# Optimization experiments

Measured on AMD Instinct MI355X. Metric: run time of the kernel, lower is better.

## Reference

```python
import jax, jax.numpy as jnp
import numpy as np

EMBED = 1024
B, S = 8, 2048

def setup_inputs() -> dict:
    key = jax.random.key(0)
    k1, k2 = jax.random.split(key)
    x = jax.random.normal(k1, (B, S, EMBED), dtype=jnp.float32)
    # torch Linear(embed, 3*embed): store weight already transposed as [E, 3E]
    W_qkv = jax.random.normal(k2, (EMBED, 3 * EMBED), dtype=jnp.float32) * (1.0 / np.sqrt(EMBED))
    b_qkv = jnp.zeros((3 * EMBED,), dtype=jnp.float32)
    return {"x": x, "W_qkv": W_qkv, "b_qkv": b_qkv}

def reference(x, W_qkv, b_qkv):
    E = x.shape[-1]
    qkv = x @ W_qkv + b_qkv                      # [B,S,3E]
    Q, K, V = jnp.split(qkv, 3, axis=-1)         # each [B,S,E]
    scale = 1.0 / jnp.sqrt(jnp.asarray(E, x.dtype))
    scores = jnp.einsum('bqe,bke->bqk', Q, K) * scale  # [B,S,S]
    attn = jax.nn.softmax(scores, axis=-1)
    return jnp.einsum('bqk,bke->bqe', attn, V)   # [B,S,E]
```

## Files before the change

kernel.cpp:

```cpp
#include <hip/hip_runtime.h>

typedef unsigned short u16;
typedef unsigned int u32;
typedef __attribute__((ext_vector_type(8))) short short8;
typedef __attribute__((ext_vector_type(4))) short short4v;
typedef __attribute__((ext_vector_type(4))) float f32x4;

__device__ __forceinline__ u16 f2bf(float f) {
    u32 u = __float_as_uint(f);
    u32 r = (u + 0x7fffu + ((u >> 16) & 1u)) >> 16;
    return (u16)r;
}
__device__ __forceinline__ float bf2f(u16 h) {
    return __uint_as_float(((u32)h) << 16);
}

__device__ __forceinline__ void gload_lds16(const void* g, void* l) {
    __builtin_amdgcn_global_load_lds((const __attribute__((address_space(1))) void*)g,
                                     (__attribute__((address_space(3))) void*)l, 16, 0, 0);
}

#define BARRIER() do { __builtin_amdgcn_sched_barrier(0); __builtin_amdgcn_s_barrier(); __builtin_amdgcn_sched_barrier(0); } while (0)
#define VMCNT(N)  asm volatile("s_waitcnt vmcnt(" #N ")" ::: "memory")

#define STAGE(ptr, LDG, LOFF, RBASE, kelem) \
    do { gload_lds16((ptr) + (size_t)(RBASE) * (LDG) + (kelem),        lds + (LOFF) + ((RBASE) + (wid << 3)) * 128); \
         gload_lds16((ptr) + (size_t)((RBASE) + 64) * (LDG) + (kelem), lds + (LOFF) + ((RBASE) + 64 + (wid << 3)) * 128); } while (0)

template<int ROFF, int QH>
__device__ __forceinline__ void ld_a(short8 (&a)[4][2], const char* lds, int arow, int c0, int c1) {
    #pragma unroll
    for (int mf = 0; mf < 4; ++mf) {
        a[mf][0] = *(const short8*)(lds + ROFF + QH * 16384 + mf * 2048 + arow + c0);
        a[mf][1] = *(const short8*)(lds + ROFF + QH * 16384 + mf * 2048 + arow + c1);
    }
}
template<int ROFF, int QH>
__device__ __forceinline__ void ld_b(short8 (&b)[2][2], const char* lds, int brow, int c0, int c1) {
    #pragma unroll
    for (int nf = 0; nf < 2; ++nf) {
        b[nf][0] = *(const short8*)(lds + ROFF + QH * 16384 + nf * 2048 + brow + c0);
        b[nf][1] = *(const short8*)(lds + ROFF + QH * 16384 + nf * 2048 + brow + c1);
    }
}

template<int QM, int QN>
__device__ __forceinline__ void mfq(f32x4 (&acc)[2][4][2][2], short8 (&a)[4][2], short8 (&b)[2][2]) {
    __builtin_amdgcn_s_setprio(1);
    #pragma unroll
    for (int mf = 0; mf < 4; ++mf)
        #pragma unroll
        for (int nf = 0; nf < 2; ++nf) {
            acc[QM][mf][QN][nf] = __builtin_amdgcn_mfma_f32_16x16x32_bf16(a[mf][0], b[nf][0], acc[QM][mf][QN][nf], 0, 0, 0);
            acc[QM][mf][QN][nf] = __builtin_amdgcn_mfma_f32_16x16x32_bf16(a[mf][1], b[nf][1], acc[QM][mf][QN][nf], 0, 0, 0);
        }
    __builtin_amdgcn_s_setprio(0);
}

template<int EPI, int LDA, int LDB, int LDC, int K>
__global__ __launch_bounds__(512, 2)
void gemm8p(const u16* __restrict__ A, long long sA,
            const u16* __restrict__ B, long long sB,
            void* __restrict__ Cv, long long sC,
            const float* __restrict__ bias, float* __restrict__ ps,
            u16* __restrict__ vt, float scale, int GX, int GY)
{
    extern __shared__ char lds[];
    const int tid  = threadIdx.x;
    const int wid  = tid >> 6;
    const int lane = tid & 63;

    const int nwg = gridDim.x;
    int bid = blockIdx.x;
    bid = (bid & 7) * (nwg >> 3) + (bid >> 3);
    const int bx  = bid % GX;
    const int rem = bid / GX;
    const int by  = rem % GY;
    const long long z = rem / GY;

    const int bm = by * 256, bn = bx * 256;
    const u16* Atile = A + z * sA + (size_t)bm * LDA;
    const u16* Btile = B + z * sB + (size_t)bn * LDB;

    const int wm = wid >> 2, wn = wid & 3;
    const int l15   = lane & 15;
    const int lxor  = (lane & 7) << 4;
    const int khi   = (lane >> 4) << 4;
    const int colk0 = khi ^ lxor;
    const int colk1 = (64 + khi) ^ lxor;
    const int arow  = (wm * 64 + l15) * 128;
    const int brow  = (wn * 32 + l15) * 128;

    const int swz = ((lane & 7) ^ (lane >> 3)) << 3;
    const u16* pA = Atile + (size_t)((wid << 3) + (lane >> 3)) * LDA + swz;
    const u16* pB = Btile + (size_t)((wid << 3) + (lane >> 3)) * LDB + swz;

    f32x4 acc[2][4][2][2];
    #pragma unroll
    for (int i = 0; i < 2; ++i)
        #pragma unroll
        for (int m = 0; m < 4; ++m)
            #pragma unroll
            for (int j = 0; j < 2; ++j)
                #pragma unroll
                for (int n = 0; n < 2; ++n)
                    acc[i][m][j][n] = (f32x4){0.f, 0.f, 0.f, 0.f};

    STAGE(pA, LDA, 0,     0,   0);  STAGE(pA, LDA, 0,     128, 0);
    STAGE(pB, LDB, 32768, 0,   0);  STAGE(pB, LDB, 32768, 128, 0);
    STAGE(pA, LDA, 65536, 0,   64);
    STAGE(pB, LDB, 98304, 0,   64); STAGE(pB, LDB, 98304, 128, 64);
    VMCNT(6);
    BARRIER();

    short8 a[4][2], b0[2][2], b1[2][2];
    const int NI = K >> 7;

    for (int it = 0; it < NI; ++it) {
        const bool more = (it + 1 < NI);
        const int kc1 = it * 128 + 64;
        const int kn  = it * 128 + 128;
        const int kn2 = kn + 64;

        ld_a<0, 0>(a, lds, arow, colk0, colk1);
        ld_b<32768, 0>(b0, lds, brow, colk0, colk1);
        STAGE(pA, LDA, 65536, 128, kc1);
        BARRIER(); mfq<0, 0>(acc, a, b0);
        ld_b<32768, 1>(b1, lds, brow, colk0, colk1);
        BARRIER(); mfq<0, 1>(acc, a, b1);
        ld_a<0, 1>(a, lds, arow, colk0, colk1);
        if (more) STAGE(pB, LDB, 32768, 0, kn);
        BARRIER(); mfq<1, 1>(acc, a, b1);
        if (more) { STAGE(pB, LDB, 32768, 128, kn); VMCNT(4); }
        else      { VMCNT(0); }
        BARRIER(); mfq<1, 0>(acc, a, b0);
        ld_a<65536, 0>(a, lds, arow, colk0, colk1);
        ld_b<98304, 0>(b0, lds, brow, colk0, colk1);
        if (more) STAGE(pA, LDA, 0, 0, kn);
        BARRIER(); mfq<0, 0>(acc, a, b0);
        ld_b<98304, 1>(b1, lds, brow, colk0, colk1);
        if (more) STAGE(pA, LDA, 0, 128, kn);
        BARRIER(); mfq<0, 1>(acc, a, b1);
        ld_a<65536, 1>(a, lds, arow, colk0, colk1);
        if (more) { STAGE(pB, LDB, 98304, 0, kn2); STAGE(pB, LDB, 98304, 128, kn2); }
        BARRIER(); mfq<1, 1>(acc, a, b1);
        if (more) STAGE(pA, LDA, 65536, 0, kn2);
        VMCNT(6);
        BARRIER(); mfq<1, 0>(acc, a, b0);
    }

    const int r0 = (lane >> 4) * 4;
    const int cc = lane & 15;

    if (EPI == 3) {
        BARRIER();
        float* rs = (float*)lds;
        u16* C = (u16*)Cv + z * sC;
        float rsum[2][4][4];
        #pragma unroll
        for (int qm = 0; qm < 2; ++qm)
            #pragma unroll
            for (int mf = 0; mf < 4; ++mf)
                #pragma unroll
                for (int r = 0; r < 4; ++r) rsum[qm][mf][r] = 0.f;
        #pragma unroll
        for (int qn = 0; qn < 2; ++qn)
            #pragma unroll
            for (int nf = 0; nf < 2; ++nf) {
                const int col = bn + qn * 128 + wn * 32 + nf * 16 + cc;
                #pragma unroll
                for (int qm = 0; qm < 2; ++qm)
                    #pragma unroll
                    for (int mf = 0; mf < 4; ++mf) {
                        const int row = bm + qm * 128 + wm * 64 + mf * 16 + r0;
                        #pragma unroll
                        for (int r = 0; r < 4; ++r) {
                            const float e = __expf(acc[qm][mf][qn][nf][r] * scale);
                            const u16 eb = f2bf(e);
                            C[(size_t)(row + r) * LDC + col] = eb;
                            rsum[qm][mf][r] += bf2f(eb);
                        }
                    }
            }
        #pragma unroll
        for (int qm = 0; qm < 2; ++qm)
            #pragma unroll
            for (int mf = 0; mf < 4; ++mf)
                #pragma unroll
                for (int r = 0; r < 4; ++r) {
                    float v = rsum[qm][mf][r];
                    v += __shfl_xor(v, 1); v += __shfl_xor(v, 2);
                    v += __shfl_xor(v, 4); v += __shfl_xor(v, 8);
                    if (cc == 0)
                        rs[wn * 256 + qm * 128 + wm * 64 + mf * 16 + r0 + r] = v;
                }
        __syncthreads();
        if (tid < 256) {
            const float s = rs[tid] + rs[256 + tid] + rs[512 + tid] + rs[768 + tid];
            ps[((size_t)z * 2048 + bm + tid) * GX + bx] = s;
        }
        return;
    }

    if (EPI == 0 && bn >= 2048) {
        #pragma unroll
        for (int qn = 0; qn < 2; ++qn)
            #pragma unroll
            for (int nf = 0; nf < 2; ++nf) {
                const int col = bn + qn * 128 + wn * 32 + nf * 16 + cc;
                const float badd = bias[col];
                const int e = col - 2048;
                #pragma unroll
                for (int qm = 0; qm < 2; ++qm)
                    #pragma unroll
                    for (int mf = 0; mf < 4; ++mf) {
                        const int row = bm + qm * 128 + wm * 64 + mf * 16 + r0;
                        short4v o;
                        #pragma unroll
                        for (int r = 0; r < 4; ++r)
                            o[r] = (short)f2bf(acc[qm][mf][qn][nf][r] + badd);
                        *(short4v*)&vt[((size_t)(row >> 11) << 21) + (size_t)e * 2048 + (row & 2047)] = o;
                    }
            }
        return;
    }

    #pragma unroll
    for (int qn = 0; qn < 2; ++qn)
        #pragma unroll
        for (int nf = 0; nf < 2; ++nf) {
            const int col = bn + qn * 128 + wn * 32 + nf * 16 + cc;
            const float badd = (EPI == 0) ? bias[col] : 0.f;
            #pragma unroll
            for (int qm = 0; qm < 2; ++qm)
                #pragma unroll
                for (int mf = 0; mf < 4; ++mf) {
                    const int row = bm + qm * 128 + wm * 64 + mf * 16 + r0;
                    #pragma unroll
                    for (int r = 0; r < 4; ++r) {
                        if (EPI == 4) {
                            const float v = acc[qm][mf][qn][nf][r] * scale *
                                            bias[(size_t)z * 2048 + row + r];
                            ((float*)Cv + z * sC)[(size_t)(row + r) * LDC + col] = v;
                        } else {
                            const float v = acc[qm][mf][qn][nf][r] * scale + badd;
                            ((u16*)Cv + z * sC)[(size_t)(row + r) * LDC + col] = f2bf(v);
                        }
                    }
                }
        }
}

__global__ __launch_bounds__(256)
void denom_inv(const float* __restrict__ Ps, float* __restrict__ dinv, int n)
{
    const int i = blockIdx.x * 256 + threadIdx.x;
    if (i >= n) return;
    const float* p = Ps + (size_t)i * 8;
    const float s = ((p[0] + p[1]) + (p[2] + p[3])) + ((p[4] + p[5]) + (p[6] + p[7]));
    dinv[i] = 1.0f / s;
}

__global__ __launch_bounds__(256)
void cvt_f32_bf16(const float* __restrict__ in, u16* __restrict__ out, int n8)
{
    const int i = blockIdx.x * 256 + threadIdx.x;
    if (i >= n8) return;
    const float4* p = (const float4*)in;
    const float4 a = p[2 * i], b = p[2 * i + 1];
    short8 o;
    o[0] = (short)f2bf(a.x); o[1] = (short)f2bf(a.y);
    o[2] = (short)f2bf(a.z); o[3] = (short)f2bf(a.w);
    o[4] = (short)f2bf(b.x); o[5] = (short)f2bf(b.y);
    o[6] = (short)f2bf(b.z); o[7] = (short)f2bf(b.w);
    ((short8*)out)[i] = o;
}

__global__ __launch_bounds__(256)
void cvt_w_t(const float* __restrict__ W, u16* __restrict__ Wt)
{
    __shared__ u16 T[32][33];
    const int tid = threadIdx.x;
    const int tr = tid >> 3;
    const int tc = (tid & 7) * 4;
    const int c0 = blockIdx.x * 32;
    const int r0 = blockIdx.y * 32;
    const float4 v = *(const float4*)&W[(size_t)(r0 + tr) * 3072 + c0 + tc];
    T[tr][tc + 0] = f2bf(v.x); T[tr][tc + 1] = f2bf(v.y);
    T[tr][tc + 2] = f2bf(v.z); T[tr][tc + 3] = f2bf(v.w);
    __syncthreads();
    short4v o;
    o[0] = (short)T[tc + 0][tr]; o[1] = (short)T[tc + 1][tr];
    o[2] = (short)T[tc + 2][tr]; o[3] = (short)T[tc + 3][tr];
    *(short4v*)&Wt[(size_t)(c0 + tr) * 1024 + r0 + tc] = o;
}

extern "C" void kernel_launch(void* const* d_in, const int* in_sizes, int n_in,
                              void* d_out, int out_size, void* d_ws, size_t ws_size,
                              hipStream_t stream) {
    const float* x    = (const float*)d_in[0];
    const float* W    = (const float*)d_in[1];
    const float* bias = (const float*)d_in[2];
    float* out = (float*)d_out;

    const int B = 8, S = 2048, E = 1024, N3 = 3072;
    const int M = B * S;

    char* ws = (char*)d_ws;
    u16* xb   = (u16*)ws;
    u16* Wtb  = (u16*)(ws + 33554432);
    u16* qkvb = (u16*)(ws + 39845888);
    u16* Vtb  = (u16*)(ws + 140509184);
    u16* Sb   = (u16*)(ws + 174063616);

    const size_t sbFull = (size_t)B * S * S * 2;
    const size_t sbOne  = (size_t)S * S * 2;
    const size_t psFull = (size_t)M * 8 * sizeof(float);
    const size_t need_full = 174063616ull + sbFull + psFull + (size_t)M * sizeof(float);
    const bool full = ws_size >= need_full;

    float* Ps   = (float*)(ws + 174063616 + (full ? sbFull : sbOne));
    float* dinv = Ps + (full ? (size_t)M * 8 : (size_t)S * 8);

    const float sc = 1.0f / 32.0f;
    const int LDSB = 131072;

    auto kQKV = gemm8p<0, 1024, 1024, 3072, 1024>;
    auto kQKT = gemm8p<3, 3072, 3072, 2048, 1024>;
    auto kPV  = gemm8p<4, 2048, 2048, 1024, 2048>;
    (void)hipFuncSetAttribute(reinterpret_cast<const void*>(kQKV),
                              hipFuncAttributeMaxDynamicSharedMemorySize, LDSB);
    (void)hipFuncSetAttribute(reinterpret_cast<const void*>(kQKT),
                              hipFuncAttributeMaxDynamicSharedMemorySize, LDSB);
    (void)hipFuncSetAttribute(reinterpret_cast<const void*>(kPV),
                              hipFuncAttributeMaxDynamicSharedMemorySize, LDSB);

    cvt_f32_bf16<<<dim3((M * E) / 8 / 256), 256, 0, stream>>>(x, xb, (M * E) / 8);
    cvt_w_t<<<dim3(96, 32), 256, 0, stream>>>(W, Wtb);

    kQKV<<<dim3(12 * 64), 512, LDSB, stream>>>(xb, 0, Wtb, 0, qkvb, 0,
                                               bias, nullptr, Vtb, 1.0f, 12, 64);

    if (full) {
        kQKT<<<dim3(8 * 8 * 8), 512, LDSB, stream>>>(
            qkvb, (long long)S * N3, qkvb + E, (long long)S * N3,
            Sb, (long long)S * S, nullptr, Ps, nullptr, sc, 8, 8);
        denom_inv<<<dim3(M / 256), 256, 0, stream>>>(Ps, dinv, M);
        kPV<<<dim3(4 * 8 * 8), 512, LDSB, stream>>>(
            Sb, (long long)S * S, Vtb, (long long)E * S,
            out, (long long)S * E, dinv, nullptr, nullptr, 1.0f, 4, 8);
    } else {
        for (int b = 0; b < B; ++b) {
            const u16* Qb = qkvb + (size_t)b * S * N3;
            kQKT<<<dim3(8 * 8), 512, LDSB, stream>>>(
                Qb, 0, Qb + E, 0, Sb, 0, nullptr, Ps, nullptr, sc, 8, 8);
            denom_inv<<<dim3(S / 256), 256, 0, stream>>>(Ps, dinv, S);
            kPV<<<dim3(4 * 8), 512, LDSB, stream>>>(
                Sb, 0, Vtb + (size_t)b * E * S, 0,
                out + (size_t)b * S * E, 0, dinv, nullptr, nullptr, 1.0f, 4, 8);
        }
    }
}
```

Measured before the change: 266.4 us.

## Restructure GEMM main loop from eight to four barrier phases per iteration

The GEMM main loop is reorganized so that each 128-wide K iteration has four barrier-separated phases instead of eight. Each phase now issues two MFMA quadrants back to back, and the global-to-LDS staging loads and vmcnt waits are reordered to match. The aim is to cut barrier synchronization overhead and give the scheduler longer MFMA runs. The cost is less interleaving of LDS reads with compute and a changed prefetch distance, which could expose load latency or create LDS hazards if the wait counts are wrong.

```diff
diff --git a/kernel.cpp b/kernel.cpp
--- a/kernel.cpp
+++ b/kernel.cpp
@@ -59,7 +59,7 @@
 
 template<int EPI, int LDA, int LDB, int LDC, int K>
 __global__ __launch_bounds__(512, 2)
-void gemm8p(const u16* __restrict__ A, long long sA,
+void gemm4p(const u16* __restrict__ A, long long sA,
             const u16* __restrict__ B, long long sB,
             void* __restrict__ Cv, long long sC,
             const float* __restrict__ bias, float* __restrict__ ps,
@@ -108,9 +108,8 @@
 
     STAGE(pA, LDA, 0,     0,   0);  STAGE(pA, LDA, 0,     128, 0);
     STAGE(pB, LDB, 32768, 0,   0);  STAGE(pB, LDB, 32768, 128, 0);
-    STAGE(pA, LDA, 65536, 0,   64);
-    STAGE(pB, LDB, 98304, 0,   64); STAGE(pB, LDB, 98304, 128, 64);
-    VMCNT(6);
+    STAGE(pA, LDA, 65536, 0,   64); STAGE(pB, LDB, 98304, 0,   64);
+    VMCNT(4);
     BARRIER();
 
     short8 a[4][2], b0[2][2], b1[2][2];
@@ -124,29 +123,26 @@
 
         ld_a<0, 0>(a, lds, arow, colk0, colk1);
         ld_b<32768, 0>(b0, lds, brow, colk0, colk1);
-        STAGE(pA, LDA, 65536, 128, kc1);
-        BARRIER(); mfq<0, 0>(acc, a, b0);
         ld_b<32768, 1>(b1, lds, brow, colk0, colk1);
-        BARRIER(); mfq<0, 1>(acc, a, b1);
+        STAGE(pB, LDB, 98304, 128, kc1); STAGE(pA, LDA, 65536, 128, kc1);
+        VMCNT(8);
+        BARRIER();
+        mfq<0, 0>(acc, a, b0); mfq<0, 1>(acc, a, b1);
         ld_a<0, 1>(a, lds, arow, colk0, colk1);
-        if (more) STAGE(pB, LDB, 32768, 0, kn);
-        BARRIER(); mfq<1, 1>(acc, a, b1);
-        if (more) { STAGE(pB, LDB, 32768, 128, kn); VMCNT(4); }
-        else      { VMCNT(0); }
-        BARRIER(); mfq<1, 0>(acc, a, b0);
+        if (more) { STAGE(pA, LDA, 0, 0, kn); STAGE(pB, LDB, 32768, 0, kn); }
+        BARRIER();
+        mfq<1, 1>(acc, a, b1); mfq<1, 0>(acc, a, b0);
         ld_a<65536, 0>(a, lds, arow, colk0, colk1);
         ld_b<98304, 0>(b0, lds, brow, colk0, colk1);
-        if (more) STAGE(pA, LDA, 0, 0, kn);
-        BARRIER(); mfq<0, 0>(acc, a, b0);
         ld_b<98304, 1>(b1, lds, brow, colk0, colk1);
-        if (more) STAGE(pA, LDA, 0, 128, kn);
-        BARRIER(); mfq<0, 1>(acc, a, b1);
+        if (more) { STAGE(pB, LDB, 32768, 128, kn); STAGE(pA, LDA, 0, 128, kn); VMCNT(8); }
+        else      { VMCNT(0); }
+        BARRIER();
+        mfq<0, 0>(acc, a, b0); mfq<0, 1>(acc, a, b1);
         ld_a<65536, 1>(a, lds, arow, colk0, colk1);
-        if (more) { STAGE(pB, LDB, 98304, 0, kn2); STAGE(pB, LDB, 98304, 128, kn2); }
-        BARRIER(); mfq<1, 1>(acc, a, b1);
-        if (more) STAGE(pA, LDA, 65536, 0, kn2);
-        VMCNT(6);
-        BARRIER(); mfq<1, 0>(acc, a, b0);
+        if (more) { STAGE(pA, LDA, 65536, 0, kn2); STAGE(pB, LDB, 98304, 0, kn2); }
+        BARRIER();
+        mfq<1, 1>(acc, a, b1); mfq<1, 0>(acc, a, b0);
     }
 
     const int r0 = (lane >> 4) * 4;
@@ -325,9 +321,9 @@
     const float sc = 1.0f / 32.0f;
     const int LDSB = 131072;
 
-    auto kQKV = gemm8p<0, 1024, 1024, 3072, 1024>;
-    auto kQKT = gemm8p<3, 3072, 3072, 2048, 1024>;
-    auto kPV  = gemm8p<4, 2048, 2048, 1024, 2048>;
+    auto kQKV = gemm4p<0, 1024, 1024, 3072, 1024>;
+    auto kQKT = gemm4p<3, 3072, 3072, 2048, 1024>;
+    auto kPV  = gemm4p<4, 2048, 2048, 1024, 2048>;
     (void)hipFuncSetAttribute(reinterpret_cast<const void*>(kQKV),
                               hipFuncAttributeMaxDynamicSharedMemorySize, LDSB);
     (void)hipFuncSetAttribute(reinterpret_cast<const void*>(kQKT),
```

Measured after the change: 269.2 us. No clear change (+1.1%).
